# Performance work log

Measured on AMD Instinct MI355X. Metric: run time of the kernel, lower is better.

Reference implementation:

```python
import jax, jax.numpy as jnp
import numpy as np
from jax import lax

B, N, T, H, C = 131072, 62, 5, 32, 3


def lstm(x, w_ih, w_hh, b_ih, b_hh):
    # x: (B, T, I); gates order i,f,g,o (PyTorch convention)
    b, t, _ = x.shape
    h_dim = w_hh.shape[1]
    xg = jnp.einsum('bti,gi->btg', x, w_ih) + b_ih + b_hh  # (B,T,4H)

    def step(carry, xg_t):
        h, c = carry
        g = xg_t + h @ w_hh.T
        i, f, gg, o = jnp.split(g, 4, axis=-1)
        c = jax.nn.sigmoid(f) * c + jax.nn.sigmoid(i) * jnp.tanh(gg)
        h = jax.nn.sigmoid(o) * jnp.tanh(c)
        return (h, c), h

    z = jnp.zeros((b, h_dim), dtype=x.dtype)
    _, hs = lax.scan(step, (z, z), xg.transpose(1, 0, 2))
    return hs.transpose(1, 0, 2)  # (B,T,H)


def ln_lrelu(x, g, b):
    # LayerNorm over last two dims (seq_len, hidden) jointly, then LeakyReLU(0.01)
    mu = x.mean(axis=(1, 2), keepdims=True)
    var = x.var(axis=(1, 2), keepdims=True)
    y = (x - mu) * lax.rsqrt(var + 1e-5) * g + b
    return jax.nn.leaky_relu(y, 0.01)


def setup_inputs() -> dict:
    key = jax.random.key(0)
    ks = jax.random.split(key, 16)
    sc = lambda fan: 1.0 / np.sqrt(H)
    d = {
        'data': jax.random.normal(ks[0], (B, 1, N, T), dtype=jnp.float32),
        'w_ih0': jax.random.uniform(ks[1], (4 * H, N), minval=-sc(N), maxval=sc(N)),
        'w_hh0': jax.random.uniform(ks[2], (4 * H, H), minval=-sc(H), maxval=sc(H)),
        'b_ih0': jax.random.uniform(ks[3], (4 * H,), minval=-sc(H), maxval=sc(H)),
        'b_hh0': jax.random.uniform(ks[4], (4 * H,), minval=-sc(H), maxval=sc(H)),
        'g0': jnp.ones((T, H), jnp.float32),
        'be0': jnp.zeros((T, H), jnp.float32),
        'w_ih1': jax.random.uniform(ks[5], (4 * H, H), minval=-sc(H), maxval=sc(H)),
        'w_hh1': jax.random.uniform(ks[6], (4 * H, H), minval=-sc(H), maxval=sc(H)),
        'b_ih1': jax.random.uniform(ks[7], (4 * H,), minval=-sc(H), maxval=sc(H)),
        'b_hh1': jax.random.uniform(ks[8], (4 * H,), minval=-sc(H), maxval=sc(H)),
        'g1': jnp.ones((T, H), jnp.float32),
        'be1': jnp.zeros((T, H), jnp.float32),
        'dw': jax.random.normal(ks[9], (C, T * H), dtype=jnp.float32) * 0.05,
        'db': jnp.zeros((C,), jnp.float32),
    }
    return d


def reference(data, w_ih0, w_hh0, b_ih0, b_hh0, g0, be0,
              w_ih1, w_hh1, b_ih1, b_hh1, g1, be1, dw, db):
    x = data.squeeze(1).transpose(0, 2, 1)  # (B, T, N)
    out0 = ln_lrelu(lstm(x, w_ih0, w_hh0, b_ih0, b_hh0), g0, be0)   # dropout=eval
    out1 = ln_lrelu(lstm(out0, w_ih1, w_hh1, b_ih1, b_hh1), g1, be1)
    out = out1 + out0  # residual
    flat = out.reshape(out.shape[0], -1)  # (B, T*H)
    return jax.nn.leaky_relu(flat @ dw.T + db, 0.01)
```

## Files before the change

### kernel.cpp

```cpp
#include <hip/hip_runtime.h>
#include <hip/hip_bf16.h>

#define THREADS 512
#define SPB 16

__device__ __forceinline__ float fsig(float x){
    return __builtin_amdgcn_rcpf(1.0f + __expf(-x));
}
__device__ __forceinline__ float ftanh(float x){
    x = fminf(fmaxf(x, -12.0f), 12.0f);
    float e = __expf(2.0f * x);
    return (e - 1.0f) * __builtin_amdgcn_rcpf(e + 1.0f);
}
__device__ __forceinline__ float lrelu(float x){
    return x > 0.0f ? x : 0.01f * x;
}

__global__ void diag_kernel(float* outp, float code){
    outp[0] = code;
}

__device__ __forceinline__ void load_wh_global(const float* __restrict__ whh, int j, float (&wh)[4][32]){
    #pragma unroll
    for (int r = 0; r < 4; ++r){
        const float* rp = whh + (r*32 + j)*32;
        #pragma unroll
        for (int q = 0; q < 8; ++q){
            float4 v = *(const float4*)(rp + q*4);
            wh[r][q*4+0] = v.x; wh[r][q*4+1] = v.y;
            wh[r][q*4+2] = v.z; wh[r][q*4+3] = v.w;
        }
    }
}

__device__ __forceinline__ void lstm_rec(const float (&wh)[4][32], const float (&acc)[5][4],
                                         float (&out)[5]){
    float h = 0.0f, c = 0.0f;
    #pragma unroll
    for (int t = 0; t < 5; ++t){
        float q0 = acc[t][0], q1 = acc[t][1], q2 = acc[t][2], q3 = acc[t][3];
        if (t > 0){
            #pragma unroll
            for (int k = 0; k < 32; ++k){
                float hk = __shfl(h, k, 32);
                q0 = fmaf(wh[0][k], hk, q0);
                q1 = fmaf(wh[1][k], hk, q1);
                q2 = fmaf(wh[2][k], hk, q2);
                q3 = fmaf(wh[3][k], hk, q3);
            }
        }
        float iv = fsig(q0), fv = fsig(q1), gv = ftanh(q2), ov = fsig(q3);
        c = fmaf(fv, c, iv * gv);
        h = ov * ftanh(c);
        out[t] = h;
    }
}

__device__ __forceinline__ void ln_lrelu(float (&o)[5], const float* gs, const float* bs, int j){
    float s1 = 0.0f, s2 = 0.0f;
    #pragma unroll
    for (int t = 0; t < 5; ++t){ s1 += o[t]; s2 = fmaf(o[t], o[t], s2); }
    #pragma unroll
    for (int m = 1; m < 32; m <<= 1){
        s1 += __shfl_xor(s1, m, 64);
        s2 += __shfl_xor(s2, m, 64);
    }
    float mu   = s1 * (1.0f/160.0f);
    float var  = s2 * (1.0f/160.0f) - mu*mu;
    float rstd = rsqrtf(var + 1e-5f);
    #pragma unroll
    for (int t = 0; t < 5; ++t){
        float y = (o[t] - mu) * rstd;
        y = fmaf(y, gs[t*32 + j], bs[t*32 + j]);
        o[t] = lrelu(y);
    }
}

__global__ __launch_bounds__(THREADS, 1)
void reslstm_kernel(const float* __restrict__ data,
                    const float* __restrict__ wih0, const float* __restrict__ whh0,
                    const float* __restrict__ bih0, const float* __restrict__ bhh0,
                    const float* __restrict__ g0p,  const float* __restrict__ be0p,
                    const float* __restrict__ wih1, const float* __restrict__ whh1,
                    const float* __restrict__ bih1, const float* __restrict__ bhh1,
                    const float* __restrict__ g1p,  const float* __restrict__ be1p,
                    const float* __restrict__ dwp,  const float* __restrict__ dbp,
                    float* __restrict__ outp, int Btot)
{
    __shared__ __attribute__((aligned(16))) float xs[SPB*320];
    __shared__ __attribute__((aligned(16))) float wbuf[128*68];
    __shared__ __attribute__((aligned(16))) float out0s[SPB*160];
    __shared__ float bias0s[128], bias1s[128];
    __shared__ float g0s[160], be0s[160], g1s[160], be1s[160];
    __shared__ float dws[480];
    __shared__ float dbs[3];

    const int tid = threadIdx.x;
    const int b0  = blockIdx.x * SPB;
    const int nsamp = (Btot - b0 < SPB) ? (Btot - b0) : SPB;

    {
        const float* dat = data + (size_t)b0 * 310;
        for (int i = tid; i < nsamp*310; i += THREADS){
            int s = i / 310, r = i - s*310;
            int n = r / 5,   t = r - n*5;
            xs[s*320 + t*64 + n] = dat[i];
        }
        for (int i = tid; i < SPB*10; i += THREADS){
            int s = i / 10, q = i - s*10;
            xs[s*320 + (q>>1)*64 + 62 + (q&1)] = 0.0f;
        }
        for (int i = tid; i < 128*62; i += THREADS){
            int row = i / 62, n = i - row*62;
            wbuf[row*68 + n] = wih0[i];
        }
        for (int i = tid; i < 128*6; i += THREADS){
            int row = i / 6, n = i - row*6;
            wbuf[row*68 + 62 + n] = 0.0f;
        }
        if (tid < 128)       bias0s[tid] = bih0[tid] + bhh0[tid];
        else if (tid < 256){ int q = tid - 128; bias1s[q] = bih1[q] + bhh1[q]; }
        else if (tid < 416){ int q = tid - 256;
            g0s[q] = g0p[q];  be0s[q] = be0p[q];
            g1s[q] = g1p[q];  be1s[q] = be1p[q];
        }
        for (int i = tid; i < 480; i += THREADS) dws[i] = dwp[i];
        if (tid < 3) dbs[tid] = dbp[tid];
    }
    __syncthreads();

    const int j = tid & 31;
    const int s = tid >> 5;

    float acc[5][4];
    #pragma unroll
    for (int r = 0; r < 4; ++r){
        float bv = bias0s[r*32 + j];
        #pragma unroll
        for (int t = 0; t < 5; ++t) acc[t][r] = bv;
    }
    {
        const float* xp  = xs   + s*320;
        const float* wp0 = wbuf + j*68;
        #pragma unroll 4
        for (int n0 = 0; n0 < 64; n0 += 4){
            float4 w[4];
            #pragma unroll
            for (int r = 0; r < 4; ++r)
                w[r] = *(const float4*)(wp0 + r*32*68 + n0);
            #pragma unroll
            for (int t = 0; t < 5; ++t){
                float4 xv = *(const float4*)(xp + t*64 + n0);
                #pragma unroll
                for (int r = 0; r < 4; ++r)
                    acc[t][r] = fmaf(w[r].x, xv.x, fmaf(w[r].y, xv.y, fmaf(w[r].z, xv.z, fmaf(w[r].w, xv.w, acc[t][r]))));
            }
        }
    }

    float o0[5];
    {
        float wh[4][32];
        load_wh_global(whh0, j, wh);
        lstm_rec(wh, acc, o0);
    }
    ln_lrelu(o0, g0s, be0s, j);
    #pragma unroll
    for (int t = 0; t < 5; ++t) out0s[s*160 + t*32 + j] = o0[t];

    __syncthreads();
    for (int i = tid; i < 128*32; i += THREADS){
        int row = i >> 5, k = i & 31;
        wbuf[row*36 + k] = wih1[i];
    }
    for (int i = tid; i < 128*4; i += THREADS){
        int row = i >> 2;
        wbuf[row*36 + 32 + (i & 3)] = 0.0f;
    }
    __syncthreads();

    #pragma unroll
    for (int r = 0; r < 4; ++r){
        float bv = bias1s[r*32 + j];
        #pragma unroll
        for (int t = 0; t < 5; ++t) acc[t][r] = bv;
    }
    {
        const float* wp1 = wbuf  + j*36;
        const float* op  = out0s + s*160;
        #pragma unroll 2
        for (int k0 = 0; k0 < 32; k0 += 4){
            float4 w[4];
            #pragma unroll
            for (int r = 0; r < 4; ++r)
                w[r] = *(const float4*)(wp1 + r*32*36 + k0);
            #pragma unroll
            for (int t = 0; t < 5; ++t){
                float4 ov = *(const float4*)(op + t*32 + k0);
                #pragma unroll
                for (int r = 0; r < 4; ++r)
                    acc[t][r] = fmaf(w[r].x, ov.x, fmaf(w[r].y, ov.y, fmaf(w[r].z, ov.z, fmaf(w[r].w, ov.w, acc[t][r]))));
            }
        }
    }

    float o1[5];
    {
        float wh[4][32];
        load_wh_global(whh1, j, wh);
        lstm_rec(wh, acc, o1);
    }
    ln_lrelu(o1, g1s, be1s, j);
    #pragma unroll
    for (int t = 0; t < 5; ++t) o1[t] += o0[t];

    float p0 = 0.0f, p1 = 0.0f, p2 = 0.0f;
    #pragma unroll
    for (int t = 0; t < 5; ++t){
        float v = o1[t];
        p0 = fmaf(dws[      t*32 + j], v, p0);
        p1 = fmaf(dws[160 + t*32 + j], v, p1);
        p2 = fmaf(dws[320 + t*32 + j], v, p2);
    }
    #pragma unroll
    for (int m = 1; m < 32; m <<= 1){
        p0 += __shfl_xor(p0, m, 64);
        p1 += __shfl_xor(p1, m, 64);
        p2 += __shfl_xor(p2, m, 64);
    }
    if (j < 3 && s < nsamp){
        float v = (j == 0) ? p0 : ((j == 1) ? p1 : p2);
        v = lrelu(v + dbs[j]);
        outp[(size_t)(b0 + s)*3 + j] = v;
    }
}

extern "C" void kernel_launch(void* const* d_in, const int* in_sizes, int n_in,
                              void* d_out, int out_size, void* d_ws, size_t ws_size,
                              hipStream_t stream)
{
    (void)d_ws; (void)ws_size;

    const int B = out_size / 3;

    int idx_data = 0;
    for (int i = 1; i < n_in; ++i)
        if (in_sizes[i] > in_sizes[idx_data]) idx_data = i;

    static const int dict_map[15]  = {0,1,2,3,4,5,6,7,8,9,10,11,12,13,14};
    static const int alpha_map[15] = {6,13,11,2,0,9,4,14,12,3,1,10,5,8,7};
    static const int rev_map[15]   = {14,13,12,11,10,9,8,7,6,5,4,3,2,1,0};

    const int* map = dict_map;
    if (idx_data == 6)       map = alpha_map;
    else if (idx_data == 14) map = rev_map;

    long ds  = (long)in_sizes[idx_data];
    long ws0 = (long)in_sizes[map[1]];
    bool ok = (ds == (long)B*310 || ds == (long)B*620 || ds == (long)B*1240)
           && (ws0 == 7936 || ws0 == 15872 || ws0 == 31744);

    if (!ok || B <= 0){
        diag_kernel<<<1, 1, 0, stream>>>((float*)d_out, 100.0f + 10.0f*idx_data);
        return;
    }

    const float* P[15];
    for (int k = 0; k < 15; ++k) P[k] = (const float*)d_in[map[k]];

    const int nblocks = (B + SPB - 1) / SPB;
    reslstm_kernel<<<dim3(nblocks), dim3(THREADS), 0, stream>>>(
        P[0], P[1], P[2], P[3], P[4], P[5], P[6], P[7], P[8], P[9],
        P[10], P[11], P[12], P[13], P[14],
        (float*)d_out, B);
}
```

Baseline: 1.071 ms.

## Read input-projection weights from global memory instead of staging them in LDS

Removes the per-block LDS staging of both layers' input-to-hidden weights, together with the two barriers around the layer-1 reload. A small prep kernel pads w_ih0 to 64 columns in the workspace so threads can read it with aligned float4 loads straight from global/L2, and w_ih1 is read directly from its input buffer. Shared memory per block drops by about 35KB and launch bounds are raised to allow four blocks per CU, aiming for higher occupancy. In exchange, weight reads now go through the cache hierarchy instead of LDS, and the register budget per thread is tighter, which could cause spills.

```diff
diff --git a/kernel.cpp b/kernel.cpp
--- a/kernel.cpp
+++ b/kernel.cpp
@@ -18,6 +18,14 @@
 
 __global__ void diag_kernel(float* outp, float code){
     outp[0] = code;
+}
+
+__global__ void prep_kernel(const float* __restrict__ wih0, float* __restrict__ wpad){
+    int i = blockIdx.x * 256 + threadIdx.x;
+    if (i < 128*64){
+        int row = i >> 6, n = i & 63;
+        wpad[i] = (n < 62) ? wih0[row*62 + n] : 0.0f;
+    }
 }
 
 __device__ __forceinline__ void load_wh_global(const float* __restrict__ whh, int j, float (&wh)[4][32]){
@@ -76,9 +84,9 @@
     }
 }
 
-__global__ __launch_bounds__(THREADS, 1)
+__global__ __launch_bounds__(THREADS, 4)
 void reslstm_kernel(const float* __restrict__ data,
-                    const float* __restrict__ wih0, const float* __restrict__ whh0,
+                    const float* __restrict__ wpad, const float* __restrict__ whh0,
                     const float* __restrict__ bih0, const float* __restrict__ bhh0,
                     const float* __restrict__ g0p,  const float* __restrict__ be0p,
                     const float* __restrict__ wih1, const float* __restrict__ whh1,
@@ -88,7 +96,6 @@
                     float* __restrict__ outp, int Btot)
 {
     __shared__ __attribute__((aligned(16))) float xs[SPB*320];
-    __shared__ __attribute__((aligned(16))) float wbuf[128*68];
     __shared__ __attribute__((aligned(16))) float out0s[SPB*160];
     __shared__ float bias0s[128], bias1s[128];
     __shared__ float g0s[160], be0s[160], g1s[160], be1s[160];
@@ -110,14 +117,6 @@
             int s = i / 10, q = i - s*10;
             xs[s*320 + (q>>1)*64 + 62 + (q&1)] = 0.0f;
         }
-        for (int i = tid; i < 128*62; i += THREADS){
-            int row = i / 62, n = i - row*62;
-            wbuf[row*68 + n] = wih0[i];
-        }
-        for (int i = tid; i < 128*6; i += THREADS){
-            int row = i / 6, n = i - row*6;
-            wbuf[row*68 + 62 + n] = 0.0f;
-        }
         if (tid < 128)       bias0s[tid] = bih0[tid] + bhh0[tid];
         else if (tid < 256){ int q = tid - 128; bias1s[q] = bih1[q] + bhh1[q]; }
         else if (tid < 416){ int q = tid - 256;
@@ -140,14 +139,14 @@
         for (int t = 0; t < 5; ++t) acc[t][r] = bv;
     }
     {
-        const float* xp  = xs   + s*320;
-        const float* wp0 = wbuf + j*68;
+        const float* xp  = xs + s*320;
+        const float* wp0 = wpad + j*64;
         #pragma unroll 4
         for (int n0 = 0; n0 < 64; n0 += 4){
             float4 w[4];
             #pragma unroll
             for (int r = 0; r < 4; ++r)
-                w[r] = *(const float4*)(wp0 + r*32*68 + n0);
+                w[r] = *(const float4*)(wp0 + r*2048 + n0);
             #pragma unroll
             for (int t = 0; t < 5; ++t){
                 float4 xv = *(const float4*)(xp + t*64 + n0);
@@ -168,17 +167,6 @@
     #pragma unroll
     for (int t = 0; t < 5; ++t) out0s[s*160 + t*32 + j] = o0[t];
 
-    __syncthreads();
-    for (int i = tid; i < 128*32; i += THREADS){
-        int row = i >> 5, k = i & 31;
-        wbuf[row*36 + k] = wih1[i];
-    }
-    for (int i = tid; i < 128*4; i += THREADS){
-        int row = i >> 2;
-        wbuf[row*36 + 32 + (i & 3)] = 0.0f;
-    }
-    __syncthreads();
-
     #pragma unroll
     for (int r = 0; r < 4; ++r){
         float bv = bias1s[r*32 + j];
@@ -186,14 +174,14 @@
         for (int t = 0; t < 5; ++t) acc[t][r] = bv;
     }
     {
-        const float* wp1 = wbuf  + j*36;
+        const float* wp1 = wih1 + j*32;
         const float* op  = out0s + s*160;
         #pragma unroll 2
         for (int k0 = 0; k0 < 32; k0 += 4){
             float4 w[4];
             #pragma unroll
             for (int r = 0; r < 4; ++r)
-                w[r] = *(const float4*)(wp1 + r*32*36 + k0);
+                w[r] = *(const float4*)(wp1 + r*1024 + k0);
             #pragma unroll
             for (int t = 0; t < 5; ++t){
                 float4 ov = *(const float4*)(op + t*32 + k0);
@@ -239,7 +227,7 @@
                               void* d_out, int out_size, void* d_ws, size_t ws_size,
                               hipStream_t stream)
 {
-    (void)d_ws; (void)ws_size;
+    (void)ws_size;
 
     const int B = out_size / 3;
 
@@ -268,9 +256,12 @@
     const float* P[15];
     for (int k = 0; k < 15; ++k) P[k] = (const float*)d_in[map[k]];
 
+    float* wpad = (float*)d_ws;
+    prep_kernel<<<dim3(32), dim3(256), 0, stream>>>(P[1], wpad);
+
     const int nblocks = (B + SPB - 1) / SPB;
     reslstm_kernel<<<dim3(nblocks), dim3(THREADS), 0, stream>>>(
-        P[0], P[1], P[2], P[3], P[4], P[5], P[6], P[7], P[8], P[9],
+        P[0], wpad, P[2], P[3], P[4], P[5], P[6], P[7], P[8], P[9],
         P[10], P[11], P[12], P[13], P[14],
         (float*)d_out, B);
 }
```

After: 2.577 ms. +140.7%, slower.
